# Optimization experiments

Hardware: AMD Instinct MI355X
Metric: run time of the kernel (lower is better)

Reference implementation:

```python
import jax, jax.numpy as jnp
import numpy as np

B, T, N, HID = 64, 24, 184, 128
IN2 = 2  # 2 * in_dim


def setup_inputs() -> dict:
    key = jax.random.key(0)
    ks = jax.random.split(key, 7)
    s = 1.0 / np.sqrt(HID)
    return {
        "pm25_hist": jax.random.normal(ks[0], (B, T, N, 1), dtype=jnp.float32),
        "W_ih": jax.random.uniform(ks[1], (3 * HID, IN2), dtype=jnp.float32, minval=-s, maxval=s),
        "W_hh": jax.random.uniform(ks[2], (3 * HID, HID), dtype=jnp.float32, minval=-s, maxval=s),
        "b_ih": jax.random.uniform(ks[3], (3 * HID,), dtype=jnp.float32, minval=-s, maxval=s),
        "b_hh": jax.random.uniform(ks[4], (3 * HID,), dtype=jnp.float32, minval=-s, maxval=s),
        "fc_w": jax.random.uniform(ks[5], (1, HID), dtype=jnp.float32, minval=-s, maxval=s),
        "fc_b": jax.random.uniform(ks[6], (1,), dtype=jnp.float32, minval=-s, maxval=s),
    }


def _encoder(pm25_hist, W_ih, W_hh, b_ih, b_hh, fc_w, fc_b):
    b, t, n, _ = pm25_hist.shape
    hid = W_hh.shape[1]
    h0 = jnp.zeros((b * n, hid), dtype=pm25_hist.dtype)
    x0 = jnp.zeros((b, n, 1), dtype=pm25_hist.dtype)
    xs = jnp.transpose(pm25_hist, (1, 0, 2, 3))  # [T, B, N, 1]

    def step(carry, pm_t):
        hn, xn = carry
        x = jnp.concatenate([xn, pm_t], axis=-1).reshape(b * n, -1)  # [B*N, 2]
        gi = x @ W_ih.T + b_ih      # [B*N, 3H]
        gh = hn @ W_hh.T + b_hh     # [B*N, 3H]
        i_r, i_z, i_n = jnp.split(gi, 3, axis=-1)
        h_r, h_z, h_n = jnp.split(gh, 3, axis=-1)
        r = jax.nn.sigmoid(i_r + h_r)
        z = jax.nn.sigmoid(i_z + h_z)
        nt = jnp.tanh(i_n + r * h_n)
        h_new = (1.0 - z) * nt + z * hn
        Ht = h_new.reshape(b, n, hid)
        x_new = Ht @ fc_w.T + fc_b  # [B, N, 1]
        return (h_new, x_new), Ht

    (_, xn_final), H = jax.lax.scan(step, (h0, x0), xs)
    H = jnp.transpose(H, (1, 0, 2, 3))  # [B, T, N, HID]
    return H, xn_final


def reference(pm25_hist, W_ih, W_hh, b_ih, b_hh, fc_w, fc_b):
    return _encoder(pm25_hist, W_ih, W_hh, b_ih, b_hh, fc_w, fc_b)
```

## Files before the change

kernel.cpp:

```cpp
#include <hip/hip_runtime.h>
#include <hip/hip_fp16.h>


#define B_   64
#define T_   24
#define N_   184
#define H_   128
#define BN   (B_ * N_)
#define TN   (T_ * N_)
#define HSZ  (B_ * T_ * N_ * H_)
#define MROWS 16
#define NBLK  (BN / MROWS)
#define S16   136

typedef _Float16 v8h __attribute__((ext_vector_type(8)));
typedef float    v4f __attribute__((ext_vector_type(4)));

static __device__ __forceinline__ float fast_rcp(float x) {
#if __has_builtin(__builtin_amdgcn_rcpf)
    return __builtin_amdgcn_rcpf(x);
#else
    return 1.0f / x;
#endif
}
static __device__ __forceinline__ float sigm_f(float x) {
    return fast_rcp(1.0f + __expf(-x));
}
static __device__ __forceinline__ float tanh_f(float x) {
    return 1.0f - 2.0f * fast_rcp(1.0f + __expf(2.0f * x));
}

__global__ __launch_bounds__(512, 4)
void gru_encoder_kernel(const float* __restrict__ pm,
                        const float* __restrict__ Wih,
                        const float* __restrict__ Whh,
                        const float* __restrict__ bih,
                        const float* __restrict__ bhh,
                        const float* __restrict__ fcw,
                        const float* __restrict__ fcb,
                        float* __restrict__ out)
{
    __shared__ _Float16 hf[2][MROWS * S16];
    __shared__ float    pml[T_ * MROWS];

    const int tid  = threadIdx.x;
    const int w    = tid >> 6;
    const int lane = tid & 63;
    const int u    = lane & 15;
    const int q    = lane >> 4;
    const int i    = w * 16 + u;

    for (int idx = tid; idx < MROWS * S16; idx += 512) hf[0][idx] = (_Float16)0.0f;

    for (int idx = tid; idx < T_ * MROWS; idx += 512) {
        const int row = idx & (MROWS - 1);
        const int t   = idx >> 4;
        const int g   = blockIdx.x * MROWS + row;
        const int b   = g / N_;
        const int n   = g - b * N_;
        pml[idx] = pm[b * TN + t * N_ + n];
    }

    v8h bfr[3][4];
#pragma unroll
    for (int g = 0; g < 3; ++g) {
        const int c = g * 128 + i;
        const float fold = (g < 2) ? Wih[c * 2 + 0] : 0.0f;
#pragma unroll
        for (int ks = 0; ks < 4; ++ks) {
            v8h hb;
#pragma unroll
            for (int j = 0; j < 8; ++j) {
                const int k = ks * 32 + q * 8 + j;
                hb[j] = (_Float16)(Whh[c * 128 + k] + fold * fcw[k]);
            }
            bfr[g][ks] = hb;
        }
    }
    v8h bfx[4];
#pragma unroll
    for (int ks = 0; ks < 4; ++ks) {
        v8h hb;
#pragma unroll
        for (int j = 0; j < 8; ++j) hb[j] = (_Float16)fcw[ks * 32 + q * 8 + j];
        bfx[ks] = hb;
    }

    const float w1r = Wih[(0 * 128 + i) * 2 + 1];
    const float w1z = Wih[(1 * 128 + i) * 2 + 1];
    const float w1n = Wih[(2 * 128 + i) * 2 + 1];
    const float w0n = Wih[(2 * 128 + i) * 2 + 0];
    const float fcbv = fcb[0];
    const float brz_r0 = bih[0 * 128 + i] + bhh[0 * 128 + i];
    const float brz_z0 = bih[1 * 128 + i] + bhh[1 * 128 + i];
    const float brz_r1 = brz_r0 + Wih[(0 * 128 + i) * 2 + 0] * fcbv;
    const float brz_z1 = brz_z0 + Wih[(1 * 128 + i) * 2 + 0] * fcbv;
    const float bin_ = bih[2 * 128 + i];
    const float bhn_ = bhh[2 * 128 + i];

    int obase[4];
#pragma unroll
    for (int reg = 0; reg < 4; ++reg) {
        const int g = blockIdx.x * MROWS + q * 4 + reg;
        const int b = g / N_;
        obase[reg] = b * TN + (g - b * N_);
    }

    v4f hreg = (v4f){0.f, 0.f, 0.f, 0.f};

    __syncthreads();

    for (int t = 0; t < T_; ++t) {
        const _Float16* hfr = hf[t & 1];
        v4f acc0 = (v4f){0.f, 0.f, 0.f, 0.f};
        v4f acc1 = (v4f){0.f, 0.f, 0.f, 0.f};
        v4f acc2 = (v4f){0.f, 0.f, 0.f, 0.f};
        v4f accx = (v4f){0.f, 0.f, 0.f, 0.f};
#pragma unroll
        for (int ks = 0; ks < 4; ++ks) {
            const v8h afr = *(const v8h*)&hfr[u * S16 + ks * 32 + q * 8];
            acc0 = __builtin_amdgcn_mfma_f32_16x16x32_f16(afr, bfr[0][ks], acc0, 0, 0, 0);
            acc1 = __builtin_amdgcn_mfma_f32_16x16x32_f16(afr, bfr[1][ks], acc1, 0, 0, 0);
            acc2 = __builtin_amdgcn_mfma_f32_16x16x32_f16(afr, bfr[2][ks], acc2, 0, 0, 0);
            accx = __builtin_amdgcn_mfma_f32_16x16x32_f16(afr, bfx[ks],    accx, 0, 0, 0);
        }

        _Float16* hfw = hf[(t + 1) & 1];
        const float brzr = (t == 0) ? brz_r0 : brz_r1;
        const float brzz = (t == 0) ? brz_z0 : brz_z1;
        const int tN = t * N_;
#pragma unroll
        for (int reg = 0; reg < 4; ++reg) {
            const int lr   = q * 4 + reg;
            const float pmv = pml[t * MROWS + lr];
            const float xv  = (t == 0) ? 0.0f : (accx[reg] + fcbv);
            const float r   = sigm_f(acc0[reg] + pmv * w1r + brzr);
            const float z   = sigm_f(acc1[reg] + pmv * w1z + brzz);
            const float nt  = tanh_f(xv * w0n + pmv * w1n + bin_ + r * (acc2[reg] + bhn_));
            const float hnew = nt + z * (hreg[reg] - nt);
            hreg[reg] = hnew;
            hfw[lr * S16 + i] = (_Float16)hnew;
            out[(size_t)(obase[reg] + tN) * H_ + i] = hnew;
        }
        __syncthreads();
    }

    if (w == 0) {
        v4f accx = (v4f){0.f, 0.f, 0.f, 0.f};
#pragma unroll
        for (int ks = 0; ks < 4; ++ks) {
            const v8h afr = *(const v8h*)&hf[0][u * S16 + ks * 32 + q * 8];
            accx = __builtin_amdgcn_mfma_f32_16x16x32_f16(afr, bfx[ks], accx, 0, 0, 0);
        }
        if (u == 0) {
#pragma unroll
            for (int reg = 0; reg < 4; ++reg)
                out[(size_t)HSZ + blockIdx.x * MROWS + q * 4 + reg] = accx[reg] + fcbv;
        }
    }
}

extern "C" void kernel_launch(void* const* d_in, const int* in_sizes, int n_in,
                              void* d_out, int out_size, void* d_ws, size_t ws_size,
                              hipStream_t stream) {
    const float* pm  = (const float*)d_in[0];
    const float* Wih = (const float*)d_in[1];
    const float* Whh = (const float*)d_in[2];
    const float* bih = (const float*)d_in[3];
    const float* bhh = (const float*)d_in[4];
    const float* fcw = (const float*)d_in[5];
    const float* fcb = (const float*)d_in[6];
    float* out = (float*)d_out;

    gru_encoder_kernel<<<dim3(NBLK), dim3(512), 0, stream>>>(
        pm, Wih, Whh, bih, bhh, fcw, fcb, out);
}
```

Before: 203.8 us.

## Process 23 rows per block with two MFMA row tiles and exp2-prescaled gates

Result: slower. 230.5 us (+13.1%).

```diff
diff --git a/kernel.cpp b/kernel.cpp
--- a/kernel.cpp
+++ b/kernel.cpp
@@ -9,7 +9,8 @@
 #define BN   (B_ * N_)
 #define TN   (T_ * N_)
 #define HSZ  (B_ * T_ * N_ * H_)
-#define MROWS 16
+#define MROWS 23
+#define RSLOT 32
 #define NBLK  (BN / MROWS)
 #define S16   136
 
@@ -23,11 +24,18 @@
     return 1.0f / x;
 #endif
 }
-static __device__ __forceinline__ float sigm_f(float x) {
-    return fast_rcp(1.0f + __expf(-x));
-}
-static __device__ __forceinline__ float tanh_f(float x) {
-    return 1.0f - 2.0f * fast_rcp(1.0f + __expf(2.0f * x));
+static __device__ __forceinline__ float fast_exp2(float x) {
+#if __has_builtin(__builtin_amdgcn_exp2f)
+    return __builtin_amdgcn_exp2f(x);
+#else
+    return __exp2f(x);
+#endif
+}
+static __device__ __forceinline__ float sigm2(float s) {
+    return fast_rcp(1.0f + fast_exp2(s));
+}
+static __device__ __forceinline__ float tanh2(float y) {
+    return 1.0f - 2.0f * fast_rcp(1.0f + fast_exp2(y));
 }
 
 __global__ __launch_bounds__(512, 4)
@@ -40,8 +48,8 @@
                         const float* __restrict__ fcb,
                         float* __restrict__ out)
 {
-    __shared__ _Float16 hf[2][MROWS * S16];
-    __shared__ float    pml[T_ * MROWS];
+    __shared__ _Float16 hf[2][RSLOT * S16];
+    __shared__ float    pml[T_ * MROWS + 16];
 
     const int tid  = threadIdx.x;
     const int w    = tid >> 6;
@@ -50,29 +58,31 @@
     const int q    = lane >> 4;
     const int i    = w * 16 + u;
 
-    for (int idx = tid; idx < MROWS * S16; idx += 512) hf[0][idx] = (_Float16)0.0f;
-
     for (int idx = tid; idx < T_ * MROWS; idx += 512) {
-        const int row = idx & (MROWS - 1);
-        const int t   = idx >> 4;
+        const int t   = idx / MROWS;
+        const int row = idx - t * MROWS;
         const int g   = blockIdx.x * MROWS + row;
         const int b   = g / N_;
-        const int n   = g - b * N_;
-        pml[idx] = pm[b * TN + t * N_ + n];
-    }
+        pml[idx] = pm[b * TN + t * N_ + (g - b * N_)];
+    }
+    if (tid < 16) pml[T_ * MROWS + tid] = 0.0f;
+
+    const float LOG2E = 1.4426950408889634f;
+    const float C2    = 2.0f * LOG2E;
 
     v8h bfr[3][4];
 #pragma unroll
     for (int g = 0; g < 3; ++g) {
         const int c = g * 128 + i;
-        const float fold = (g < 2) ? Wih[c * 2 + 0] : 0.0f;
+        const float fold  = (g < 2) ? Wih[c * 2 + 0] : 0.0f;
+        const float scale = (g < 2) ? -LOG2E : C2;
 #pragma unroll
         for (int ks = 0; ks < 4; ++ks) {
             v8h hb;
 #pragma unroll
             for (int j = 0; j < 8; ++j) {
                 const int k = ks * 32 + q * 8 + j;
-                hb[j] = (_Float16)(Whh[c * 128 + k] + fold * fcw[k]);
+                hb[j] = (_Float16)(scale * (Whh[c * 128 + k] + fold * fcw[k]));
             }
             bfr[g][ks] = hb;
         }
@@ -86,76 +96,109 @@
         bfx[ks] = hb;
     }
 
-    const float w1r = Wih[(0 * 128 + i) * 2 + 1];
-    const float w1z = Wih[(1 * 128 + i) * 2 + 1];
-    const float w1n = Wih[(2 * 128 + i) * 2 + 1];
-    const float w0n = Wih[(2 * 128 + i) * 2 + 0];
     const float fcbv = fcb[0];
-    const float brz_r0 = bih[0 * 128 + i] + bhh[0 * 128 + i];
-    const float brz_z0 = bih[1 * 128 + i] + bhh[1 * 128 + i];
-    const float brz_r1 = brz_r0 + Wih[(0 * 128 + i) * 2 + 0] * fcbv;
-    const float brz_z1 = brz_z0 + Wih[(1 * 128 + i) * 2 + 0] * fcbv;
-    const float bin_ = bih[2 * 128 + i];
-    const float bhn_ = bhh[2 * 128 + i];
-
-    int obase[4];
-#pragma unroll
-    for (int reg = 0; reg < 4; ++reg) {
-        const int g = blockIdx.x * MROWS + q * 4 + reg;
-        const int b = g / N_;
-        obase[reg] = b * TN + (g - b * N_);
-    }
-
-    v4f hreg = (v4f){0.f, 0.f, 0.f, 0.f};
+    const float w1r  = -LOG2E * Wih[(0 * 128 + i) * 2 + 1];
+    const float w1z  = -LOG2E * Wih[(1 * 128 + i) * 2 + 1];
+    const float w1n  = C2 * Wih[(2 * 128 + i) * 2 + 1];
+    const float w0n  = C2 * Wih[(2 * 128 + i) * 2 + 0];
+    const float brz_r0 = -LOG2E * (bih[0 * 128 + i] + bhh[0 * 128 + i]);
+    const float brz_z0 = -LOG2E * (bih[1 * 128 + i] + bhh[1 * 128 + i]);
+    const float brz_r1 = brz_r0 - LOG2E * Wih[(0 * 128 + i) * 2 + 0] * fcbv;
+    const float brz_z1 = brz_z0 - LOG2E * Wih[(1 * 128 + i) * 2 + 0] * fcbv;
+    const float bin_ = C2 * bih[2 * 128 + i];
+    const float bhn_ = C2 * bhh[2 * 128 + i];
+
+    int obase[2][4];
+#pragma unroll
+    for (int rt = 0; rt < 2; ++rt)
+#pragma unroll
+        for (int reg = 0; reg < 4; ++reg) {
+            const int lr = rt * 16 + q * 4 + reg;
+            if (lr < MROWS) {
+                const int g = blockIdx.x * MROWS + lr;
+                const int b = g / N_;
+                obase[rt][reg] = b * TN + (g - b * N_);
+            } else {
+                obase[rt][reg] = -1;
+            }
+        }
+
+    v4f hreg[2];
+    hreg[0] = (v4f){0.f, 0.f, 0.f, 0.f};
+    hreg[1] = (v4f){0.f, 0.f, 0.f, 0.f};
 
     __syncthreads();
 
-    for (int t = 0; t < T_; ++t) {
+#pragma unroll
+    for (int rt = 0; rt < 2; ++rt) {
+#pragma unroll
+        for (int reg = 0; reg < 4; ++reg) {
+            const int lr   = rt * 16 + q * 4 + reg;
+            const float pmv = pml[lr];
+            const float r  = sigm2(pmv * w1r + brz_r0);
+            const float z  = sigm2(pmv * w1z + brz_z0);
+            const float nt = tanh2(pmv * w1n + bin_ + r * bhn_);
+            const float hnew = nt - z * nt;
+            hreg[rt][reg] = hnew;
+            hf[1][lr * S16 + i] = (_Float16)hnew;
+            const int ob = obase[rt][reg];
+            if (ob >= 0) out[(size_t)ob * H_ + i] = hnew;
+        }
+    }
+    __syncthreads();
+
+    for (int t = 1; t < T_; ++t) {
         const _Float16* hfr = hf[t & 1];
-        v4f acc0 = (v4f){0.f, 0.f, 0.f, 0.f};
-        v4f acc1 = (v4f){0.f, 0.f, 0.f, 0.f};
-        v4f acc2 = (v4f){0.f, 0.f, 0.f, 0.f};
+        _Float16*       hfw = hf[(t + 1) & 1];
+        const int tN = t * N_;
+#pragma unroll
+        for (int rt = 0; rt < 2; ++rt) {
+            v4f acc0 = (v4f){0.f, 0.f, 0.f, 0.f};
+            v4f acc1 = (v4f){0.f, 0.f, 0.f, 0.f};
+            v4f acc2 = (v4f){0.f, 0.f, 0.f, 0.f};
+            v4f accx = (v4f){0.f, 0.f, 0.f, 0.f};
+#pragma unroll
+            for (int ks = 0; ks < 4; ++ks) {
+                const v8h afr = *(const v8h*)&hfr[(rt * 16 + u) * S16 + ks * 32 + q * 8];
+                acc0 = __builtin_amdgcn_mfma_f32_16x16x32_f16(afr, bfr[0][ks], acc0, 0, 0, 0);
+                acc1 = __builtin_amdgcn_mfma_f32_16x16x32_f16(afr, bfr[1][ks], acc1, 0, 0, 0);
+                acc2 = __builtin_amdgcn_mfma_f32_16x16x32_f16(afr, bfr[2][ks], acc2, 0, 0, 0);
+                accx = __builtin_amdgcn_mfma_f32_16x16x32_f16(afr, bfx[ks],    accx, 0, 0, 0);
+            }
+#pragma unroll
+            for (int reg = 0; reg < 4; ++reg) {
+                const int lr   = rt * 16 + q * 4 + reg;
+                const float pmv = pml[t * MROWS + lr];
+                const float xv  = accx[reg] + fcbv;
+                const float r   = sigm2(acc0[reg] + pmv * w1r + brz_r1);
+                const float z   = sigm2(acc1[reg] + pmv * w1z + brz_z1);
+                const float nt  = tanh2(xv * w0n + pmv * w1n + bin_ +
+                                        r * (acc2[reg] + bhn_));
+                const float hnew = nt + z * (hreg[rt][reg] - nt);
+                hreg[rt][reg] = hnew;
+                hfw[lr * S16 + i] = (_Float16)hnew;
+                const int ob = obase[rt][reg];
+                if (ob >= 0) out[(size_t)(ob + tN) * H_ + i] = hnew;
+            }
+        }
+        __syncthreads();
+    }
+
+    if (w < 2) {
+        const int rt = w;
         v4f accx = (v4f){0.f, 0.f, 0.f, 0.f};
 #pragma unroll
         for (int ks = 0; ks < 4; ++ks) {
-            const v8h afr = *(const v8h*)&hfr[u * S16 + ks * 32 + q * 8];
-            acc0 = __builtin_amdgcn_mfma_f32_16x16x32_f16(afr, bfr[0][ks], acc0, 0, 0, 0);
-            acc1 = __builtin_amdgcn_mfma_f32_16x16x32_f16(afr, bfr[1][ks], acc1, 0, 0, 0);
-            acc2 = __builtin_amdgcn_mfma_f32_16x16x32_f16(afr, bfr[2][ks], acc2, 0, 0, 0);
-            accx = __builtin_amdgcn_mfma_f32_16x16x32_f16(afr, bfx[ks],    accx, 0, 0, 0);
-        }
-
-        _Float16* hfw = hf[(t + 1) & 1];
-        const float brzr = (t == 0) ? brz_r0 : brz_r1;
-        const float brzz = (t == 0) ? brz_z0 : brz_z1;
-        const int tN = t * N_;
-#pragma unroll
-        for (int reg = 0; reg < 4; ++reg) {
-            const int lr   = q * 4 + reg;
-            const float pmv = pml[t * MROWS + lr];
-            const float xv  = (t == 0) ? 0.0f : (accx[reg] + fcbv);
-            const float r   = sigm_f(acc0[reg] + pmv * w1r + brzr);
-            const float z   = sigm_f(acc1[reg] + pmv * w1z + brzz);
-            const float nt  = tanh_f(xv * w0n + pmv * w1n + bin_ + r * (acc2[reg] + bhn_));
-            const float hnew = nt + z * (hreg[reg] - nt);
-            hreg[reg] = hnew;
-            hfw[lr * S16 + i] = (_Float16)hnew;
-            out[(size_t)(obase[reg] + tN) * H_ + i] = hnew;
-        }
-        __syncthreads();
-    }
-
-    if (w == 0) {
-        v4f accx = (v4f){0.f, 0.f, 0.f, 0.f};
-#pragma unroll
-        for (int ks = 0; ks < 4; ++ks) {
-            const v8h afr = *(const v8h*)&hf[0][u * S16 + ks * 32 + q * 8];
+            const v8h afr = *(const v8h*)&hf[0][(rt * 16 + u) * S16 + ks * 32 + q * 8];
             accx = __builtin_amdgcn_mfma_f32_16x16x32_f16(afr, bfx[ks], accx, 0, 0, 0);
         }
         if (u == 0) {
 #pragma unroll
-            for (int reg = 0; reg < 4; ++reg)
-                out[(size_t)HSZ + blockIdx.x * MROWS + q * 4 + reg] = accx[reg] + fcbv;
+            for (int reg = 0; reg < 4; ++reg) {
+                const int lr = rt * 16 + q * 4 + reg;
+                if (lr < MROWS)
+                    out[(size_t)HSZ + blockIdx.x * MROWS + lr] = accx[reg] + fcbv;
+            }
         }
     }
 }
```
